# Kernel tuning notes

Measured on AMD Instinct MI355X. Metric: run time of the kernel, lower is better.

Reference implementation:

```python
import jax, jax.numpy as jnp
import numpy as np

K_TOP = 2          # hardcoded k in MyAttentionFunction
S = 32             # hardcoded spatial size (interpolate to 32x32)
N = S * S          # 1024 patches (patch_size=1, stride=1 unfold)
NEG = jnp.float32(-1e30)  # stand-in for excluding columns from top-k


def setup_inputs() -> dict:
    key = jax.random.key(0)
    k1, k2, k3 = jax.random.split(key, 3)
    C = 4096
    generated = jax.random.normal(k1, (1, C, S, S), dtype=jnp.float32)
    known = jax.random.normal(k2, (1, C, S, S), dtype=jnp.float32)
    mask = jax.random.randint(k3, (1, 1, S, S), 0, 2).astype(jnp.float32)
    return {"generated": generated, "known": known, "mask": mask}


def _forward(generated, known, mask):
    C = generated.shape[1]
    # F.interpolate(mask, (32,32)) nearest, then flatten -> flag in {0,1}, shape (N,)
    flag = jax.image.resize(mask, (1, 1, S, S), method="nearest").reshape(N)
    # MyUnfold(x, 1, 1) == [1, N, C]; drop batch dim of 1.
    P = generated.reshape(C, N).T   # (N, C) patches of `generated`
    Kp = known.reshape(C, N).T      # (N, C) patches of `known`

    norm_p = jnp.sum(P * P, axis=-1)   # (N,)
    norm_k = jnp.sum(Kp * Kp, axis=-1)
    # Full cosine matrices; original restricts rows to flag==1 and columns to
    # flag==0 (cosine0) / flag==1 (cosine1) by extraction; we mask columns with
    # a very negative value so top-k returns the same values with GLOBAL indices
    # (which is exactly what the original reconstructs via nonzero()[indexes]).
    cos0 = (P @ Kp.T) / jnp.sqrt(norm_p[:, None] * norm_k[None, :])  # (N, N)
    cos1 = (P @ P.T) / jnp.sqrt(norm_p[:, None] * norm_p[None, :])
    cos0 = jnp.where(flag[None, :] == 0, cos0, NEG)
    cos1 = jnp.where(flag[None, :] == 1, cos1, NEG)

    w0, i0 = jax.lax.top_k(cos0, K_TOP)  # (N, k) values / global indices
    w1, i1 = jax.lax.top_k(cos1, K_TOP)

    m = flag                      # 1.0 on masked rows
    nm = jnp.sum(m)               # number of masked patches
    # weight means taken only over masked rows, then softmax (original uses
    # .item() + numpy softmax, i.e. detached constants).
    means = jnp.stack(
        [jnp.sum(w0[:, i] * m) / nm for i in range(K_TOP)]
        + [jnp.sum(w1[:, i] * m) / nm for i in range(K_TOP)]
    )
    weights = jax.lax.stop_gradient(jax.nn.softmax(means))  # (2k,)

    # The original builds dense 1024x1024 indicator matrices and bmm's them;
    # each indicator row for a masked patch is one-hot at its retrieved source,
    # so the bmm is just a gather into masked rows. The advanced-indexing quirk
    # ind[mask_idx, src_idx] (nonzero() pairs include a leading 0 column) also
    # unconditionally sets ind[0,0]=1; we reproduce that (set semantics: no
    # double count if row 0 already maps to column 0).
    rtn = jnp.zeros((N, C), dtype=generated.dtype)
    for i in range(2 * K_TOP):
        src = Kp if i < K_TOP else P
        cols = (i0 if i < K_TOP else i1)[:, i % K_TOP]  # (N,) global indices
        out_i = jnp.where(m[:, None] == 1, src[cols], 0.0)  # masked rows only
        dup = 1.0 - ((m[0] == 1) & (cols[0] == 0)).astype(src.dtype)
        out_i = out_i.at[0].add(src[0] * dup)  # spurious ind[0,0]=1 artifact
        rtn = rtn + weights[i] * out_i

    rtn = rtn.reshape(1, S, S, C).transpose(0, 3, 1, 2)  # (1, C, 32, 32)
    return jnp.concatenate([generated, known, rtn], axis=1)


def reference(generated, known, mask):
    return _forward(generated, known, mask)
```

## Files before the change

### kernel.cpp

```cpp
#include <hip/hip_runtime.h>
#include <hip/hip_bf16.h>
#include <math.h>

#define N_TOT 1024
#define C_DIM 4096
#define T_MARGIN 3e-4f

typedef __attribute__((ext_vector_type(8))) _Float16 half8;
typedef __attribute__((ext_vector_type(8))) unsigned short ushort8;
typedef __attribute__((ext_vector_type(8))) char schar8;
typedef __attribute__((ext_vector_type(4))) float floatx4;

__device__ inline unsigned short f2h(float v) {
    _Float16 h = (_Float16)v;
    return __builtin_bit_cast(unsigned short, h);
}
__device__ inline float h2f(unsigned short u) {
    return (float)__builtin_bit_cast(_Float16, u);
}
__device__ inline char lo_enc(float v, unsigned short h) {
    int e = (h >> 10) & 31;
    float lo = v - h2f(h);
    float q = rintf(lo * 240.0f * __uint_as_float((unsigned)(152 - e) << 23));
    q = fmaxf(-127.0f, fminf(127.0f, q));
    return (char)(int)q;
}
__device__ inline float lo_dec(char q, unsigned short h) {
    int e = (h >> 10) & 31;
    return (float)q * __uint_as_float((unsigned)(e + 102) << 23) * (1.0f / 240.0f);
}

__device__ inline void ins2(float v, int s, float& v1, int& s1, float& v2, int& s2) {
    if (v > v1 || (v == v1 && s < s1)) { v2 = v1; s2 = s1; v1 = v; s1 = s; }
    else if (v > v2 || (v == v2 && s < s2)) { v2 = v; s2 = s; }
}

__global__ __launch_bounds__(256) void split_norms(const float* __restrict__ G,
                                                   const float* __restrict__ Kn,
                                                   const float* __restrict__ flag,
                                                   unsigned short* __restrict__ Phi,
                                                   char* __restrict__ Plo,
                                                   unsigned short* __restrict__ Khi,
                                                   char* __restrict__ Klo,
                                                   float* __restrict__ normP,
                                                   float* __restrict__ normK,
                                                   int* __restrict__ colidx,
                                                   int* __restrict__ n0p) {
    const int z = blockIdx.z;
    const float* X = z ? Kn : G;
    unsigned short* Xhi = z ? Khi : Phi;
    char* Xlo = z ? Klo : Plo;
    float* normX = z ? normK : normP;

    __shared__ float tile[64 * 65];
    __shared__ float np[256];
    const int t  = threadIdx.x;
    const int c0 = blockIdx.x * 64;
    const int n0 = blockIdx.y * 64;

    float s2 = 0.0f;
    #pragma unroll
    for (int s = 0; s < 16; s++) {
        int c_loc = s * 4 + (t >> 6);
        int n_loc = t & 63;
        float v = X[(c0 + c_loc) * N_TOT + n0 + n_loc];
        tile[c_loc * 65 + n_loc] = v;
        s2 = fmaf(v, v, s2);
    }
    np[t] = s2;
    __syncthreads();

    if (t < 64) {
        float tot = np[t] + np[t + 64] + np[t + 128] + np[t + 192];
        atomicAdd(&normX[n0 + t], tot);
    }

    #pragma unroll
    for (int s = 0; s < 2; s++) {
        int n_loc = s * 32 + (t >> 3);
        int c8    = (t & 7) * 8;
        unsigned short h[8]; char l[8];
        #pragma unroll
        for (int e = 0; e < 8; e++) {
            float v = tile[(c8 + e) * 65 + n_loc];
            h[e] = f2h(v);
            l[e] = lo_enc(v, h[e]);
        }
        size_t base = (size_t)(n0 + n_loc) * C_DIM + c0 + c8;
        ushort8 hv; schar8 lv;
        #pragma unroll
        for (int e = 0; e < 8; e++) { hv[e] = h[e]; lv[e] = l[e]; }
        *(ushort8*)&Xhi[base] = hv;
        *(schar8*)&Xlo[base]  = lv;
    }

    if (blockIdx.x == 0 && blockIdx.y == 0 && blockIdx.z == 0) {
        __shared__ int cz[256];
        __shared__ int co[256];
        float4 fv = *(const float4*)&flag[4 * t];
        int f[4] = {fv.x == 0.0f, fv.y == 0.0f, fv.z == 0.0f, fv.w == 0.0f};
        int nz = f[0] + f[1] + f[2] + f[3];
        cz[t] = nz; co[t] = 4 - nz;
        __syncthreads();
        for (int off = 1; off < 256; off <<= 1) {
            int vz = (t >= off) ? cz[t - off] : 0;
            int vo = (t >= off) ? co[t - off] : 0;
            __syncthreads();
            cz[t] += vz; co[t] += vo;
            __syncthreads();
        }
        const int fn0 = cz[255];
        int zs = cz[t] - nz;
        int os = fn0 + co[t] - (4 - nz);
        #pragma unroll
        for (int e = 0; e < 4; e++) {
            int j = 4 * t + e;
            if (f[e]) colidx[zs++] = j;
            else      colidx[os++] = j;
        }
        if (t == 0) *n0p = fn0;
    }
}

__global__ __launch_bounds__(256, 4) void gemm_coarse(const unsigned short* __restrict__ Phi,
                                                      const unsigned short* __restrict__ Khi,
                                                      const int* __restrict__ colidx,
                                                      const int* __restrict__ n0p,
                                                      float* __restrict__ dotPart) {
    __shared__ unsigned short sA[64 * 64];
    __shared__ unsigned short sB[128 * 64];

    const int t    = threadIdx.x;
    const int wave = t >> 6, lane = t & 63;
    const int wm   = wave >> 1, wn = wave & 1;
    const int quad = lane >> 4, lrow = lane & 15;
    const int ib = blockIdx.x * 64, jb = blockIdx.y * 128;
    const int bz = blockIdx.z;
    const int k_beg = bz * 512;
    const int n0 = *n0p;

    const int srow = t >> 3;
    const int g    = (t & 7) ^ (srow & 7);

    const unsigned short* gA[2];
    gA[0] = Phi + (size_t)(ib + srow) * C_DIM + g * 8;
    gA[1] = gA[0] + (size_t)32 * C_DIM;
    const unsigned short* gB[4];
    #pragma unroll
    for (int q = 0; q < 4; q++) {
        int s = jb + q * 32 + srow;
        int row = colidx[s];
        const unsigned short* src = (s < n0) ? Khi : Phi;
        gB[q] = src + (size_t)row * C_DIM + g * 8;
    }

    floatx4 acc[2][4] = {};

    for (int k0 = k_beg; k0 < k_beg + 512; k0 += 64) {
        #pragma unroll
        for (int q = 0; q < 2; q++)
            __builtin_amdgcn_global_load_lds(
                (const __attribute__((address_space(1))) void*)(gA[q] + k0),
                (__attribute__((address_space(3))) void*)((char*)sA + q * 4096 + t * 16), 16, 0, 0);
        #pragma unroll
        for (int q = 0; q < 4; q++)
            __builtin_amdgcn_global_load_lds(
                (const __attribute__((address_space(1))) void*)(gB[q] + k0),
                (__attribute__((address_space(3))) void*)((char*)sB + q * 4096 + t * 16), 16, 0, 0);
        __syncthreads();

        #pragma unroll
        for (int kk = 0; kk < 2; kk++) {
            const int gk = kk * 4 + quad;
            half8 a[2], b[4];
            #pragma unroll
            for (int ti = 0; ti < 2; ti++) {
                int m = wm * 32 + ti * 16 + lrow;
                a[ti] = *(const half8*)&sA[m * 64 + ((gk ^ (m & 7)) << 3)];
            }
            #pragma unroll
            for (int tj = 0; tj < 4; tj++) {
                int n = wn * 64 + tj * 16 + lrow;
                b[tj] = *(const half8*)&sB[n * 64 + ((gk ^ (n & 7)) << 3)];
            }
            #pragma unroll
            for (int ti = 0; ti < 2; ti++)
                #pragma unroll
                for (int tj = 0; tj < 4; tj++)
                    acc[ti][tj] = __builtin_amdgcn_mfma_f32_16x16x32_f16(a[ti], b[tj], acc[ti][tj], 0, 0, 0);
        }
        __syncthreads();
    }

    float* outp = dotPart + ((size_t)bz << 20);
    #pragma unroll
    for (int tj = 0; tj < 4; tj++) {
        int j = jb + wn * 64 + tj * 16 + lrow;
        #pragma unroll
        for (int ti = 0; ti < 2; ti++) {
            #pragma unroll
            for (int reg = 0; reg < 4; reg++) {
                int i = ib + wm * 32 + ti * 16 + quad * 4 + reg;
                outp[i * N_TOT + j] = acc[ti][tj][reg];
            }
        }
    }
}

__global__ __launch_bounds__(256) void select_k(const float* __restrict__ dotPart,
                                                const float* __restrict__ normP,
                                                const float* __restrict__ normK,
                                                const int* __restrict__ colidx,
                                                const int* __restrict__ n0p,
                                                float* __restrict__ w01,
                                                int* __restrict__ i01,
                                                int* __restrict__ wl_hdr,
                                                int* __restrict__ wl_cand) {
    __shared__ float sr_v1[2][4], sr_v2[2][4];
    __shared__ int   sr_s1[2][4], sr_s2[2][4];
    __shared__ int   s_cnt[2];
    __shared__ int   s_cand[2][16];

    const int row = blockIdx.x;
    const int t   = threadIdx.x;
    const int wave = t >> 6, lane = t & 63;
    const int n0 = *n0p;
    const float nr = normP[row];

    if (t < 2) s_cnt[t] = 0;

    const float* base = dotPart + (size_t)row * N_TOT + 4 * t;
    float4 p0 = *(const float4*)(base);
    float4 p1 = *(const float4*)(base + (1ull << 20));
    float4 p2 = *(const float4*)(base + (2ull << 20));
    float4 p3 = *(const float4*)(base + (3ull << 20));
    float4 p4 = *(const float4*)(base + (4ull << 20));
    float4 p5 = *(const float4*)(base + (5ull << 20));
    float4 p6 = *(const float4*)(base + (6ull << 20));
    float4 p7 = *(const float4*)(base + (7ull << 20));
    float4 dv;
    dv.x = ((p0.x + p1.x) + (p2.x + p3.x)) + ((p4.x + p5.x) + (p6.x + p7.x));
    dv.y = ((p0.y + p1.y) + (p2.y + p3.y)) + ((p4.y + p5.y) + (p6.y + p7.y));
    dv.z = ((p0.z + p1.z) + (p2.z + p3.z)) + ((p4.z + p5.z) + (p6.z + p7.z));
    dv.w = ((p0.w + p1.w) + (p2.w + p3.w)) + ((p4.w + p5.w) + (p6.w + p7.w));

    float cv[4];
    #pragma unroll
    for (int e = 0; e < 4; e++) {
        int s = 4 * t + e;
        int gj = colidx[s];
        float nb = (s < n0) ? normK[gj] : normP[gj];
        float d  = (e == 0) ? dv.x : (e == 1) ? dv.y : (e == 2) ? dv.z : dv.w;
        cv[e] = d * rsqrtf(nr * nb);
    }

    #pragma unroll
    for (int zz = 0; zz < 2; zz++) {
        float v1 = -INFINITY, v2 = -INFINITY;
        int   s1 = 0x7FFFFFFF, s2 = 0x7FFFFFFF;
        #pragma unroll
        for (int e = 0; e < 4; e++) {
            int s = 4 * t + e;
            bool inz = zz ? (s >= n0) : (s < n0);
            if (inz) ins2(cv[e], s, v1, s1, v2, s2);
        }
        #pragma unroll
        for (int off = 32; off > 0; off >>= 1) {
            float o1 = __shfl_xor(v1, off); int q1 = __shfl_xor(s1, off);
            float o2 = __shfl_xor(v2, off); int q2 = __shfl_xor(s2, off);
            ins2(o1, q1, v1, s1, v2, s2);
            ins2(o2, q2, v1, s1, v2, s2);
        }
        if (lane == 0) {
            sr_v1[zz][wave] = v1; sr_s1[zz][wave] = s1;
            sr_v2[zz][wave] = v2; sr_s2[zz][wave] = s2;
        }
    }
    __syncthreads();

    float m1z[2], m2z[2]; int b1z[2], b2z[2];
    #pragma unroll
    for (int zz = 0; zz < 2; zz++) {
        float m1 = -INFINITY, m2 = -INFINITY;
        int   b1 = 0x7FFFFFFF, b2 = 0x7FFFFFFF;
        #pragma unroll
        for (int w = 0; w < 4; w++) {
            ins2(sr_v1[zz][w], sr_s1[zz][w], m1, b1, m2, b2);
            ins2(sr_v2[zz][w], sr_s2[zz][w], m1, b1, m2, b2);
        }
        m1z[zz] = m1; m2z[zz] = m2; b1z[zz] = b1; b2z[zz] = b2;
        const float thr = m2 - T_MARGIN;
        #pragma unroll
        for (int e = 0; e < 4; e++) {
            int s = 4 * t + e;
            bool inz = zz ? (s >= n0) : (s < n0);
            if (inz && cv[e] > thr) {
                int idx = atomicAdd(&s_cnt[zz], 1);
                if (idx < 16) s_cand[zz][idx] = s;
            }
        }
    }
    __syncthreads();

    bool need[2]; int cntz[2];
    #pragma unroll
    for (int zz = 0; zz < 2; zz++) {
        const int cnt = min(s_cnt[zz], 16);
        cntz[zz] = cnt;
        const bool trusted = (s_cnt[zz] == 2) && (m1z[zz] - m2z[zz] > T_MARGIN);
        need[zz] = !trusted;
        if (t == 0) {
            wl_hdr[2 * row + zz] = trusted ? 0 : cnt;
            if (trusted) {
                int base2 = (zz * N_TOT + row) * 2;
                w01[base2]     = m1z[zz];
                w01[base2 + 1] = m2z[zz];
                i01[base2]     = colidx[b1z[zz]];
                i01[base2 + 1] = colidx[b2z[zz]];
            }
        }
    }
    __syncthreads();

    #pragma unroll
    for (int zz = 0; zz < 2; zz++)
        if (need[zz] && t < cntz[zz])
            wl_cand[(2 * row + zz) * 16 + t] = s_cand[zz][t];
}

__global__ __launch_bounds__(256) void refine2(const unsigned short* __restrict__ Phi,
                                               const char* __restrict__ Plo,
                                               const unsigned short* __restrict__ Khi,
                                               const char* __restrict__ Klo,
                                               const float* __restrict__ normP,
                                               const float* __restrict__ normK,
                                               const int* __restrict__ colidx,
                                               const int* __restrict__ n0p,
                                               const int* __restrict__ wl_hdr,
                                               const int* __restrict__ wl_cand,
                                               float* __restrict__ w01,
                                               int* __restrict__ i01) {
    __shared__ float sAf[C_DIM];
    __shared__ float s_rcv[16];
    __shared__ int   s_rcj[16];

    const int item = blockIdx.x;
    const int cnt  = wl_hdr[item];
    if (cnt == 0) return;

    const int row = item >> 1;
    const int zz  = item & 1;
    const int t   = threadIdx.x;
    const int grp = t >> 5, l32 = t & 31;
    const int n0 = *n0p;
    const float nr = normP[row];

    {
        const unsigned short* Ah = Phi + (size_t)row * C_DIM;
        const char*           Al = Plo + (size_t)row * C_DIM;
        #pragma unroll
        for (int s = 0; s < 2; s++) {
            int c = t * 16 + s * 8;
            ushort8 hb = *(const ushort8*)&Ah[c];
            schar8  lb = *(const schar8*)&Al[c];
            #pragma unroll
            for (int e = 0; e < 8; e++) sAf[c + e] = h2f(hb[e]) + lo_dec(lb[e], hb[e]);
        }
    }
    __syncthreads();

    #pragma unroll
    for (int p = 0; p < 2; p++) {
        if (p == 1 && cnt <= 8) break;
        const int q = grp + 8 * p;
        float acc = 0.0f;
        int gj = 0; float nb = 1.0f;
        if (q < cnt) {
            const int cs = wl_cand[item * 16 + q];
            gj = colidx[cs];
            nb = (cs < n0) ? normK[gj] : normP[gj];
            const unsigned short* bh_row = ((cs < n0) ? Khi : Phi) + (size_t)gj * C_DIM;
            const char*           bl_row = ((cs < n0) ? Klo : Plo) + (size_t)gj * C_DIM;
            #pragma unroll 4
            for (int it = 0; it < 16; it++) {
                int c = it * 256 + l32 * 8;
                ushort8 hb = *(const ushort8*)&bh_row[c];
                schar8  lb = *(const schar8*)&bl_row[c];
                #pragma unroll
                for (int e = 0; e < 8; e++)
                    acc = fmaf(sAf[c + e], h2f(hb[e]) + lo_dec(lb[e], hb[e]), acc);
            }
        }
        #pragma unroll
        for (int off = 16; off > 0; off >>= 1) acc += __shfl_xor(acc, off);
        if (l32 == 0 && q < cnt) {
            s_rcv[q] = acc * rsqrtf(nr * nb);
            s_rcj[q] = gj;
        }
    }
    __syncthreads();

    if (t == 0) {
        float v1 = -INFINITY, v2 = -INFINITY;
        int   j1 = 0x7FFFFFFF, j2 = 0x7FFFFFFF;
        for (int q = 0; q < cnt; q++) {
            float cvx = s_rcv[q];
            int   j   = s_rcj[q];
            if (cvx > v1 || (cvx == v1 && j < j1)) {
                v2 = v1; j2 = j1; v1 = cvx; j1 = j;
            } else if (cvx > v2 || (cvx == v2 && j < j2)) {
                v2 = cvx; j2 = j;
            }
        }
        if (j1 == 0x7FFFFFFF) j1 = 0;
        if (j2 == 0x7FFFFFFF) j2 = j1;
        int base = (zz * N_TOT + row) * 2;
        w01[base]     = v1;
        w01[base + 1] = v2;
        i01[base]     = j1;
        i01[base + 1] = j2;
    }
}

__global__ __launch_bounds__(256) void means_k(const float* __restrict__ flag,
                                               const float* __restrict__ w01,
                                               float* __restrict__ wts) {
    __shared__ float red[5][4];
    const int t = threadIdx.x;
    const int wave = t >> 6, lane = t & 63;

    float pm[5] = {};
    #pragma unroll
    for (int e = 0; e < 4; e++) {
        int n = 4 * t + e;
        float m = flag[n];
        pm[0] += m;
        pm[1] += m * w01[n * 2 + 0];
        pm[2] += m * w01[n * 2 + 1];
        pm[3] += m * w01[2 * N_TOT + n * 2 + 0];
        pm[4] += m * w01[2 * N_TOT + n * 2 + 1];
    }
    #pragma unroll
    for (int i = 0; i < 5; i++)
        #pragma unroll
        for (int off = 32; off > 0; off >>= 1)
            pm[i] += __shfl_xor(pm[i], off);
    if (lane == 0) {
        #pragma unroll
        for (int i = 0; i < 5; i++) red[i][wave] = pm[i];
    }
    __syncthreads();
    if (t == 0) {
        float tot[5];
        #pragma unroll
        for (int i = 0; i < 5; i++)
            tot[i] = red[i][0] + red[i][1] + red[i][2] + red[i][3];
        float inv = 1.0f / tot[0];
        float mv[4] = {tot[1] * inv, tot[2] * inv, tot[3] * inv, tot[4] * inv};
        float mx = fmaxf(fmaxf(mv[0], mv[1]), fmaxf(mv[2], mv[3]));
        float e[4], s = 0.0f;
        #pragma unroll
        for (int q = 0; q < 4; q++) { e[q] = expf(mv[q] - mx); s += e[q]; }
        #pragma unroll
        for (int q = 0; q < 4; q++) wts[q] = e[q] / s;
    }
}

__global__ __launch_bounds__(256) void output_kernel(const float* __restrict__ G,
                                                     const float* __restrict__ Kn,
                                                     const float* __restrict__ flag,
                                                     const int* __restrict__ i01,
                                                     const float* __restrict__ wts,
                                                     float* __restrict__ out) {
    __shared__ float sG[N_TOT];
    __shared__ float sKn[N_TOT];
    __shared__ float swts[4];
    const int c  = blockIdx.x;
    const int t  = threadIdx.x;
    const int n4 = t * 4;

    if (t < 4) swts[t] = wts[t];

    float4 gv = *(const float4*)&G[c * N_TOT + n4];
    float4 kv = *(const float4*)&Kn[c * N_TOT + n4];
    *(float4*)&sG[n4]  = gv;
    *(float4*)&sKn[n4] = kv;
    *(float4*)&out[c * N_TOT + n4] = gv;
    *(float4*)&out[C_DIM * N_TOT + c * N_TOT + n4] = kv;

    float4 fv = *(const float4*)&flag[n4];
    const float fa[4] = {fv.x, fv.y, fv.z, fv.w};
    __syncthreads();

    const float w0 = swts[0], w1 = swts[1], w2 = swts[2], w3 = swts[3];

    float val[4];
    #pragma unroll
    for (int e = 0; e < 4; e++) {
        int n = n4 + e;
        float v = 0.0f;
        if (fa[e] == 1.0f) {
            int2 i0 = *(const int2*)&i01[n * 2];
            int2 i1 = *(const int2*)&i01[2 * N_TOT + n * 2];
            v = w0 * sKn[i0.x] + w1 * sKn[i0.y]
              + w2 * sG[i1.x]  + w3 * sG[i1.y];
        }
        if (n == 0) {
            bool m0 = (flag[0] == 1.0f);
            int2 i0 = *(const int2*)&i01[0];
            int2 i1 = *(const int2*)&i01[2 * N_TOT];
            float kn0 = sKn[0];
            float g0  = sG[0];
            if (!(m0 && i0.x == 0)) v += w0 * kn0;
            if (!(m0 && i0.y == 0)) v += w1 * kn0;
            if (!(m0 && i1.x == 0)) v += w2 * g0;
            if (!(m0 && i1.y == 0)) v += w3 * g0;
        }
        val[e] = v;
    }
    *(float4*)&out[2 * C_DIM * N_TOT + c * N_TOT + n4] =
        make_float4(val[0], val[1], val[2], val[3]);
}

extern "C" void kernel_launch(void* const* d_in, const int* in_sizes, int n_in,
                              void* d_out, int out_size, void* d_ws, size_t ws_size,
                              hipStream_t stream) {
    const float* G    = (const float*)d_in[0];
    const float* Kn   = (const float*)d_in[1];
    const float* flag = (const float*)d_in[2];
    float* out = (float*)d_out;

    char* p = (char*)d_ws;
    unsigned short* Phi = (unsigned short*)p;  p += (size_t)N_TOT * C_DIM * 2;
    unsigned short* Khi = (unsigned short*)p;  p += (size_t)N_TOT * C_DIM * 2;
    char* Plo = p;                             p += (size_t)N_TOT * C_DIM;
    char* Klo = p;                             p += (size_t)N_TOT * C_DIM;
    float* dotPart = (float*)p;                p += (size_t)8 * N_TOT * N_TOT * 4;
    float* normP   = (float*)p;                p += N_TOT * 4;
    float* normK   = (float*)p;                p += N_TOT * 4;
    float* wts     = (float*)p;                p += 16;
    float* w01     = (float*)p;                p += 4 * N_TOT * 4;
    int*   i01     = (int*)p;                  p += 4 * N_TOT * 4;
    int*   colidx  = (int*)p;                  p += N_TOT * 4;
    int*   n0p     = (int*)p;                  p += 16;
    int*   wl_hdr  = (int*)p;                  p += 2 * N_TOT * 4;
    int*   wl_cand = (int*)p;

    hipMemsetAsync(normP, 0, 2 * N_TOT * sizeof(float), stream);

    split_norms<<<dim3(64, 16, 2), 256, 0, stream>>>(G, Kn, flag, Phi, Plo, Khi, Klo,
                                                     normP, normK, colidx, n0p);
    gemm_coarse<<<dim3(16, 8, 8), 256, 0, stream>>>(Phi, Khi, colidx, n0p, dotPart);
    select_k<<<1024, 256, 0, stream>>>(dotPart, normP, normK, colidx, n0p,
                                       w01, i01, wl_hdr, wl_cand);
    refine2<<<2048, 256, 0, stream>>>(Phi, Plo, Khi, Klo, normP, normK, colidx, n0p,
                                      wl_hdr, wl_cand, w01, i01);
    means_k<<<1, 256, 0, stream>>>(flag, w01, wts);
    output_kernel<<<4096, 256, 0, stream>>>(G, Kn, flag, i01, wts, out);
}
```

Before: 168.7 us.

## Enlarge GEMM tile to 128x128, vectorize split loads, process two channels per output block

The coarse GEMM block tile grows from 64x128 to 128x128, with each wave computing 4x4 MFMA tiles. This raises operand reuse per LDS load but halves the block count and lowers occupancy via launch bounds. split_norms now loads the input with float4 reads and computes the squared norms during the conversion pass using a shuffle reduction, removing a shared-memory reduction stage. The output kernel handles two channels per block so the index and flag loads are shared between them.

```diff
diff --git a/kernel.cpp b/kernel.cpp
--- a/kernel.cpp
+++ b/kernel.cpp
@@ -53,39 +53,40 @@
     float* normX = z ? normK : normP;
 
     __shared__ float tile[64 * 65];
-    __shared__ float np[256];
     const int t  = threadIdx.x;
     const int c0 = blockIdx.x * 64;
     const int n0 = blockIdx.y * 64;
 
-    float s2 = 0.0f;
-    #pragma unroll
-    for (int s = 0; s < 16; s++) {
-        int c_loc = s * 4 + (t >> 6);
-        int n_loc = t & 63;
-        float v = X[(c0 + c_loc) * N_TOT + n0 + n_loc];
-        tile[c_loc * 65 + n_loc] = v;
-        s2 = fmaf(v, v, s2);
-    }
-    np[t] = s2;
-    __syncthreads();
-
-    if (t < 64) {
-        float tot = np[t] + np[t + 64] + np[t + 128] + np[t + 192];
-        atomicAdd(&normX[n0 + t], tot);
-    }
+    #pragma unroll
+    for (int s = 0; s < 4; s++) {
+        int c_loc = s * 16 + (t >> 4);
+        int n4    = (t & 15) * 4;
+        float4 v = *(const float4*)&X[(size_t)(c0 + c_loc) * N_TOT + n0 + n4];
+        tile[c_loc * 65 + n4 + 0] = v.x;
+        tile[c_loc * 65 + n4 + 1] = v.y;
+        tile[c_loc * 65 + n4 + 2] = v.z;
+        tile[c_loc * 65 + n4 + 3] = v.w;
+    }
+    __syncthreads();
 
     #pragma unroll
     for (int s = 0; s < 2; s++) {
         int n_loc = s * 32 + (t >> 3);
         int c8    = (t & 7) * 8;
         unsigned short h[8]; char l[8];
+        float s2 = 0.0f;
         #pragma unroll
         for (int e = 0; e < 8; e++) {
             float v = tile[(c8 + e) * 65 + n_loc];
+            s2 = fmaf(v, v, s2);
             h[e] = f2h(v);
             l[e] = lo_enc(v, h[e]);
         }
+        s2 += __shfl_xor(s2, 1);
+        s2 += __shfl_xor(s2, 2);
+        s2 += __shfl_xor(s2, 4);
+        if ((t & 7) == 0) atomicAdd(&normX[n0 + n_loc], s2);
+
         size_t base = (size_t)(n0 + n_loc) * C_DIM + c0 + c8;
         ushort8 hv; schar8 lv;
         #pragma unroll
@@ -122,19 +123,19 @@
     }
 }
 
-__global__ __launch_bounds__(256, 4) void gemm_coarse(const unsigned short* __restrict__ Phi,
+__global__ __launch_bounds__(256, 2) void gemm_coarse(const unsigned short* __restrict__ Phi,
                                                       const unsigned short* __restrict__ Khi,
                                                       const int* __restrict__ colidx,
                                                       const int* __restrict__ n0p,
                                                       float* __restrict__ dotPart) {
-    __shared__ unsigned short sA[64 * 64];
+    __shared__ unsigned short sA[128 * 64];
     __shared__ unsigned short sB[128 * 64];
 
     const int t    = threadIdx.x;
     const int wave = t >> 6, lane = t & 63;
     const int wm   = wave >> 1, wn = wave & 1;
     const int quad = lane >> 4, lrow = lane & 15;
-    const int ib = blockIdx.x * 64, jb = blockIdx.y * 128;
+    const int ib = blockIdx.x * 128, jb = blockIdx.y * 128;
     const int bz = blockIdx.z;
     const int k_beg = bz * 512;
     const int n0 = *n0p;
@@ -142,9 +143,7 @@
     const int srow = t >> 3;
     const int g    = (t & 7) ^ (srow & 7);
 
-    const unsigned short* gA[2];
-    gA[0] = Phi + (size_t)(ib + srow) * C_DIM + g * 8;
-    gA[1] = gA[0] + (size_t)32 * C_DIM;
+    const unsigned short* gA0 = Phi + (size_t)(ib + srow) * C_DIM + g * 8;
     const unsigned short* gB[4];
     #pragma unroll
     for (int q = 0; q < 4; q++) {
@@ -154,13 +153,13 @@
         gB[q] = src + (size_t)row * C_DIM + g * 8;
     }
 
-    floatx4 acc[2][4] = {};
+    floatx4 acc[4][4] = {};
 
     for (int k0 = k_beg; k0 < k_beg + 512; k0 += 64) {
         #pragma unroll
-        for (int q = 0; q < 2; q++)
+        for (int q = 0; q < 4; q++)
             __builtin_amdgcn_global_load_lds(
-                (const __attribute__((address_space(1))) void*)(gA[q] + k0),
+                (const __attribute__((address_space(1))) void*)(gA0 + (size_t)q * 32 * C_DIM + k0),
                 (__attribute__((address_space(3))) void*)((char*)sA + q * 4096 + t * 16), 16, 0, 0);
         #pragma unroll
         for (int q = 0; q < 4; q++)
@@ -172,10 +171,10 @@
         #pragma unroll
         for (int kk = 0; kk < 2; kk++) {
             const int gk = kk * 4 + quad;
-            half8 a[2], b[4];
+            half8 a[4], b[4];
             #pragma unroll
-            for (int ti = 0; ti < 2; ti++) {
-                int m = wm * 32 + ti * 16 + lrow;
+            for (int ti = 0; ti < 4; ti++) {
+                int m = wm * 64 + ti * 16 + lrow;
                 a[ti] = *(const half8*)&sA[m * 64 + ((gk ^ (m & 7)) << 3)];
             }
             #pragma unroll
@@ -184,7 +183,7 @@
                 b[tj] = *(const half8*)&sB[n * 64 + ((gk ^ (n & 7)) << 3)];
             }
             #pragma unroll
-            for (int ti = 0; ti < 2; ti++)
+            for (int ti = 0; ti < 4; ti++)
                 #pragma unroll
                 for (int tj = 0; tj < 4; tj++)
                     acc[ti][tj] = __builtin_amdgcn_mfma_f32_16x16x32_f16(a[ti], b[tj], acc[ti][tj], 0, 0, 0);
@@ -197,10 +196,10 @@
     for (int tj = 0; tj < 4; tj++) {
         int j = jb + wn * 64 + tj * 16 + lrow;
         #pragma unroll
-        for (int ti = 0; ti < 2; ti++) {
+        for (int ti = 0; ti < 4; ti++) {
             #pragma unroll
             for (int reg = 0; reg < 4; reg++) {
-                int i = ib + wm * 32 + ti * 16 + quad * 4 + reg;
+                int i = ib + wm * 64 + ti * 16 + quad * 4 + reg;
                 outp[i * N_TOT + j] = acc[ti][tj][reg];
             }
         }
@@ -472,21 +471,25 @@
                                                      const int* __restrict__ i01,
                                                      const float* __restrict__ wts,
                                                      float* __restrict__ out) {
-    __shared__ float sG[N_TOT];
-    __shared__ float sKn[N_TOT];
+    __shared__ float sG[2][N_TOT];
+    __shared__ float sKn[2][N_TOT];
     __shared__ float swts[4];
-    const int c  = blockIdx.x;
+    const int c0 = blockIdx.x * 2;
     const int t  = threadIdx.x;
     const int n4 = t * 4;
 
     if (t < 4) swts[t] = wts[t];
 
-    float4 gv = *(const float4*)&G[c * N_TOT + n4];
-    float4 kv = *(const float4*)&Kn[c * N_TOT + n4];
-    *(float4*)&sG[n4]  = gv;
-    *(float4*)&sKn[n4] = kv;
-    *(float4*)&out[c * N_TOT + n4] = gv;
-    *(float4*)&out[C_DIM * N_TOT + c * N_TOT + n4] = kv;
+    #pragma unroll
+    for (int ch = 0; ch < 2; ch++) {
+        int c = c0 + ch;
+        float4 gv = *(const float4*)&G[c * N_TOT + n4];
+        float4 kv = *(const float4*)&Kn[c * N_TOT + n4];
+        *(float4*)&sG[ch][n4]  = gv;
+        *(float4*)&sKn[ch][n4] = kv;
+        *(float4*)&out[c * N_TOT + n4] = gv;
+        *(float4*)&out[C_DIM * N_TOT + c * N_TOT + n4] = kv;
+    }
 
     float4 fv = *(const float4*)&flag[n4];
     const float fa[4] = {fv.x, fv.y, fv.z, fv.w};
@@ -494,32 +497,34 @@
 
     const float w0 = swts[0], w1 = swts[1], w2 = swts[2], w3 = swts[3];
 
-    float val[4];
+    float val[2][4];
     #pragma unroll
     for (int e = 0; e < 4; e++) {
         int n = n4 + e;
-        float v = 0.0f;
+        float v0 = 0.0f, v1 = 0.0f;
         if (fa[e] == 1.0f) {
             int2 i0 = *(const int2*)&i01[n * 2];
             int2 i1 = *(const int2*)&i01[2 * N_TOT + n * 2];
-            v = w0 * sKn[i0.x] + w1 * sKn[i0.y]
-              + w2 * sG[i1.x]  + w3 * sG[i1.y];
+            v0 = w0 * sKn[0][i0.x] + w1 * sKn[0][i0.y]
+               + w2 * sG[0][i1.x]  + w3 * sG[0][i1.y];
+            v1 = w0 * sKn[1][i0.x] + w1 * sKn[1][i0.y]
+               + w2 * sG[1][i1.x]  + w3 * sG[1][i1.y];
         }
         if (n == 0) {
             bool m0 = (flag[0] == 1.0f);
             int2 i0 = *(const int2*)&i01[0];
             int2 i1 = *(const int2*)&i01[2 * N_TOT];
-            float kn0 = sKn[0];
-            float g0  = sG[0];
-            if (!(m0 && i0.x == 0)) v += w0 * kn0;
-            if (!(m0 && i0.y == 0)) v += w1 * kn0;
-            if (!(m0 && i1.x == 0)) v += w2 * g0;
-            if (!(m0 && i1.y == 0)) v += w3 * g0;
-        }
-        val[e] = v;
-    }
-    *(float4*)&out[2 * C_DIM * N_TOT + c * N_TOT + n4] =
-        make_float4(val[0], val[1], val[2], val[3]);
+            if (!(m0 && i0.x == 0)) { v0 += w0 * sKn[0][0]; v1 += w0 * sKn[1][0]; }
+            if (!(m0 && i0.y == 0)) { v0 += w1 * sKn[0][0]; v1 += w1 * sKn[1][0]; }
+            if (!(m0 && i1.x == 0)) { v0 += w2 * sG[0][0];  v1 += w2 * sG[1][0]; }
+            if (!(m0 && i1.y == 0)) { v0 += w3 * sG[0][0];  v1 += w3 * sG[1][0]; }
+        }
+        val[0][e] = v0; val[1][e] = v1;
+    }
+    #pragma unroll
+    for (int ch = 0; ch < 2; ch++)
+        *(float4*)&out[2 * C_DIM * N_TOT + (c0 + ch) * N_TOT + n4] =
+            make_float4(val[ch][0], val[ch][1], val[ch][2], val[ch][3]);
 }
 
 extern "C" void kernel_launch(void* const* d_in, const int* in_sizes, int n_in,
@@ -550,11 +555,11 @@
 
     split_norms<<<dim3(64, 16, 2), 256, 0, stream>>>(G, Kn, flag, Phi, Plo, Khi, Klo,
                                                      normP, normK, colidx, n0p);
-    gemm_coarse<<<dim3(16, 8, 8), 256, 0, stream>>>(Phi, Khi, colidx, n0p, dotPart);
+    gemm_coarse<<<dim3(8, 8, 8), 256, 0, stream>>>(Phi, Khi, colidx, n0p, dotPart);
     select_k<<<1024, 256, 0, stream>>>(dotPart, normP, normK, colidx, n0p,
                                        w01, i01, wl_hdr, wl_cand);
     refine2<<<2048, 256, 0, stream>>>(Phi, Plo, Khi, Klo, normP, normK, colidx, n0p,
                                       wl_hdr, wl_cand, w01, i01);
     means_k<<<1, 256, 0, stream>>>(flag, w01, wts);
-    output_kernel<<<4096, 256, 0, stream>>>(G, Kn, flag, i01, wts, out);
-}
+    output_kernel<<<2048, 256, 0, stream>>>(G, Kn, flag, i01, wts, out);
+}
```

Result: no change. 167.3 us (-0.8%).
